# Optimization experiments

Hardware: AMD Instinct MI355X
Metric: run time of the kernel (lower is better)

## Reference

```python
import jax, jax.numpy as jnp
import numpy as np

B, S, H, KVH, D, MD = 4, 4096, 2, 1, 2, 5  # batch, seq, heads, kv heads, head_dim, model_dim
EPS, SCALE = 1e-6, 16.0


def _rmsnorm(t):
    # RMSNormNoWeight with scale=16.0 over last dim
    var = jnp.mean(t * t, axis=-1, keepdims=True)
    return SCALE * t * jax.lax.rsqrt(var + EPS)


def _rope(t, cos, sin):
    # t: (B, S, h, D); cos/sin: (S, D//2). Complex multiply on interleaved pairs.
    tr, ti = t[..., 0::2], t[..., 1::2]
    c = cos[None, :, None, :]
    s = sin[None, :, None, :]
    out_r = tr * c - ti * s
    out_i = tr * s + ti * c
    return jnp.stack([out_r, out_i], axis=-1).reshape(t.shape)


def setup_inputs() -> dict:
    key = jax.random.key(0)
    ks = jax.random.split(key, 9)
    return {
        "x": jax.random.normal(ks[0], (B, S, MD), jnp.float32),
        "freqs": jax.random.normal(ks[1], (S, D // 2), jnp.float32),
        "shared_qk_v": jax.random.normal(ks[2], (MD,), jnp.float32),
        "shared_v_v": jax.random.normal(ks[3], (MD,), jnp.float32),
        "shared_o_v": jax.random.normal(ks[4], (H * D,), jnp.float32),
        "shared_vproj_u": jax.random.normal(ks[5], (KVH * D,), jnp.float32),
        "q_u": jax.random.normal(ks[6], (H * D,), jnp.float32),
        "k_u": jax.random.normal(ks[7], (KVH * D,), jnp.float32),
        "o_u": jax.random.normal(ks[8], (MD,), jnp.float32),
    }


def reference(x, freqs, shared_qk_v, shared_v_v, shared_o_v, shared_vproj_u, q_u, k_u, o_u):
    b, s = x.shape[0], x.shape[1]
    # rank-1 projections: (x . v) outer u
    s_qk = jnp.sum(x * shared_qk_v, axis=-1, keepdims=True)  # (B,S,1) shared by q and k
    q = (s_qk * q_u).reshape(b, s, H, D)
    k = (s_qk * k_u).reshape(b, s, KVH, D)
    s_v = jnp.sum(x * shared_v_v, axis=-1, keepdims=True)
    v = (s_v * shared_vproj_u).reshape(b, s, KVH, D)
    # qk-norm + rotary
    q = _rmsnorm(q)
    k = _rmsnorm(k)
    cos, sin = jnp.cos(freqs), jnp.sin(freqs)
    q = _rope(q, cos, sin)
    k = _rope(k, cos, sin)
    # (B,h,S,D)
    q = q.transpose(0, 2, 1, 3)
    k = k.transpose(0, 2, 1, 3)
    v = v.transpose(0, 2, 1, 3)
    # GQA repeat kv heads
    k = jnp.repeat(k, H // KVH, axis=1)
    v = jnp.repeat(v, H // KVH, axis=1)
    scores = jnp.einsum('bhqd,bhkd->bhqk', q, k) / jnp.sqrt(jnp.float32(D))
    probs = jax.nn.softmax(scores, axis=-1)
    out = jnp.einsum('bhqk,bhkd->bhqd', probs, v)
    out = out.transpose(0, 2, 1, 3).reshape(b, s, H * D)
    # rank-1 output projection
    s_o = jnp.sum(out * shared_o_v, axis=-1, keepdims=True)
    return s_o * o_u  # (B,S,MODEL_DIM)
```

## Files before the change

kernel.cpp:

```cpp
#include <hip/hip_runtime.h>
#include <math.h>


#define BQ 4
#define SQ 4096
#define MDQ 5
#define EPSQ 1e-6f
#define SCALEQ 16.0f

#define BLOCK 256
#define ROWS 32
#define SPLIT 8
#define JSUB (SQ / SPLIT)
#define TILES (SQ / ROWS)

__global__ __launch_bounds__(BLOCK)
void ca_kernel(const float* __restrict__ x,
               const float* __restrict__ freqs,
               const float* __restrict__ qk_v,
               const float* __restrict__ v_v,
               const float* __restrict__ o_v,
               const float* __restrict__ vproj_u,
               const float* __restrict__ q_u,
               const float* __restrict__ k_u,
               const float* __restrict__ o_u,
               float* __restrict__ out)
{
    __shared__ float2 sPQ[SQ];
    __shared__ float  sCv[SQ];
    __shared__ float  sRed[ROWS][SPLIT][2][3];

    const int tid  = threadIdx.x;
    const int bx   = blockIdx.x;
    const int b    = bx / TILES;
    const int tile = bx % TILES;

    const float w0 = k_u[0], w1 = k_u[1];
    const float mk = 0.5f * (w0 * w0 + w1 * w1);

    const float qk0 = qk_v[0], qk1 = qk_v[1], qk2 = qk_v[2], qk3 = qk_v[3], qk4 = qk_v[4];
    const float vv0 = v_v[0],  vv1 = v_v[1],  vv2 = v_v[2],  vv3 = v_v[3],  vv4 = v_v[4];

    for (int k = 0; k < SQ / BLOCK; ++k) {
        const int j = tid + k * BLOCK;
        const float* xr = x + (size_t)(b * SQ + j) * MDQ;
        const float x0 = xr[0], x1 = xr[1], x2 = xr[2], x3 = xr[3], x4 = xr[4];
        const float a  = x0*qk0 + x1*qk1 + x2*qk2 + x3*qk3 + x4*qk4;
        const float sv = x0*vv0 + x1*vv1 + x2*vv2 + x3*vv3 + x4*vv4;
        float sj, cj;
        __sincosf(freqs[j], &sj, &cj);
        const float mu = SCALEQ * a * rsqrtf(a * a * mk + EPSQ);
        sPQ[j] = make_float2(mu * cj, mu * sj);
        sCv[j] = sv;
    }

    const int row = tid & (ROWS - 1);
    const int sp  = tid / ROWS;
    const int i   = tile * ROWS + row;

    const float u00 = q_u[0], u01 = q_u[1], u10 = q_u[2], u11 = q_u[3];
    const float m0 = 0.5f * (u00 * u00 + u01 * u01);
    const float m1 = 0.5f * (u10 * u10 + u11 * u11);
    const float A0 = u00 * w0 + u01 * w1, B0 = u01 * w0 - u00 * w1;
    const float A1 = u10 * w0 + u11 * w1, B1 = u11 * w0 - u10 * w1;

    const float* xi = x + (size_t)(b * SQ + i) * MDQ;
    const float ai = xi[0]*qk0 + xi[1]*qk1 + xi[2]*qk2 + xi[3]*qk3 + xi[4]*qk4;
    float si, ci;
    __sincosf(freqs[i], &si, &ci);
    const float lam0 = SCALEQ * ai * rsqrtf(ai * ai * m0 + EPSQ);
    const float lam1 = SCALEQ * ai * rsqrtf(ai * ai * m1 + EPSQ);
    const float isq2 = 0.70710678118654752f;
    const float al0 = lam0 * (A0 * ci - B0 * si) * isq2;
    const float be0 = lam0 * (A0 * si + B0 * ci) * isq2;
    const float al1 = lam1 * (A1 * ci - B1 * si) * isq2;
    const float be1 = lam1 * (A1 * si + B1 * ci) * isq2;

    __syncthreads();

    const float2* __restrict__ pq  = sPQ + sp * JSUB;
    const float*  __restrict__ cvp = sCv + sp * JSUB;

    float mx0 = -1e30f, mx1 = -1e30f;
#pragma unroll 8
    for (int jj = 0; jj < JSUB; ++jj) {
        const float2 v = pq[jj];
        const float sc0 = al0 * v.x + be0 * v.y;
        const float sc1 = al1 * v.x + be1 * v.y;
        mx0 = fmaxf(mx0, sc0);
        mx1 = fmaxf(mx1, sc1);
    }

    float l0 = 0.f, n0 = 0.f, l1 = 0.f, n1 = 0.f;
#pragma unroll 4
    for (int jj = 0; jj < JSUB; ++jj) {
        const float2 v = pq[jj];
        const float cv = cvp[jj];
        const float e0 = __expf(al0 * v.x + be0 * v.y - mx0);
        const float e1 = __expf(al1 * v.x + be1 * v.y - mx1);
        l0 += e0; n0 = fmaf(e0, cv, n0);
        l1 += e1; n1 = fmaf(e1, cv, n1);
    }

    sRed[row][sp][0][0] = mx0; sRed[row][sp][0][1] = l0; sRed[row][sp][0][2] = n0;
    sRed[row][sp][1][0] = mx1; sRed[row][sp][1][1] = l1; sRed[row][sp][1][2] = n1;
    __syncthreads();

    if (tid < ROWS) {
        float W[2];
#pragma unroll
        for (int h = 0; h < 2; ++h) {
            float m = -1e30f;
#pragma unroll
            for (int s = 0; s < SPLIT; ++s) m = fmaxf(m, sRed[tid][s][h][0]);
            float l = 0.f, n = 0.f;
#pragma unroll
            for (int s = 0; s < SPLIT; ++s) {
                const float c = __expf(sRed[tid][s][h][0] - m);
                l = fmaf(sRed[tid][s][h][1], c, l);
                n = fmaf(sRed[tid][s][h][2], c, n);
            }
            W[h] = n / l;
        }
        const float p0 = vproj_u[0], p1 = vproj_u[1];
        const float d0 = p0 * o_v[0] + p1 * o_v[1];
        const float d1 = p0 * o_v[2] + p1 * o_v[3];
        const float so = W[0] * d0 + W[1] * d1;

        const int ig = tile * ROWS + tid;
        float* orow = out + (size_t)(b * SQ + ig) * MDQ;
        orow[0] = so * o_u[0];
        orow[1] = so * o_u[1];
        orow[2] = so * o_u[2];
        orow[3] = so * o_u[3];
        orow[4] = so * o_u[4];
    }
}

extern "C" void kernel_launch(void* const* d_in, const int* in_sizes, int n_in,
                              void* d_out, int out_size, void* d_ws, size_t ws_size,
                              hipStream_t stream) {
    (void)in_sizes; (void)n_in; (void)d_ws; (void)ws_size; (void)out_size;
    const float* x       = (const float*)d_in[0];
    const float* freqs   = (const float*)d_in[1];
    const float* qk_v    = (const float*)d_in[2];
    const float* v_v     = (const float*)d_in[3];
    const float* o_v     = (const float*)d_in[4];
    const float* vproj_u = (const float*)d_in[5];
    const float* q_u     = (const float*)d_in[6];
    const float* k_u     = (const float*)d_in[7];
    const float* o_u     = (const float*)d_in[8];
    float* out = (float*)d_out;

    dim3 grid(BQ * TILES);
    dim3 block(BLOCK);
    hipLaunchKernelGGL(ca_kernel, grid, block, 0, stream,
                       x, freqs, qk_v, v_v, o_v, vproj_u, q_u, k_u, o_u, out);
}
```

Baseline: 112.9 us.

## Replace max pass with analytic score bound, precompute keys in a prep kernel

The per-row max pass is dropped. It is replaced by an analytic upper bound on the scores (|q|·max|k| from the rmsnorm magnitude), so the softmax becomes a single exp2 pass with the log2e factor folded into the coefficients. A separate prep kernel writes the per-key rotated values and V scalars to workspace as float4, so each main block reads them from global/L2 instead of recomputing all 4096 keys into shared memory. The tiling changes to 16 rows by 16 splits, and a fallback single-kernel path is kept for when the workspace is too small. The risk is that the bound-based shift can underflow the exps, and it adds a second launch plus global-memory traffic.

```diff
diff --git a/kernel.cpp b/kernel.cpp
--- a/kernel.cpp
+++ b/kernel.cpp
@@ -7,42 +7,174 @@
 #define MDQ 5
 #define EPSQ 1e-6f
 #define SCALEQ 16.0f
+#define L2E 1.4426950408889634f
+#define ISQ2 0.70710678118654752f
+
+__device__ __forceinline__ float fast_exp2(float x) {
+#if __has_builtin(__builtin_amdgcn_exp2f)
+    return __builtin_amdgcn_exp2f(x);
+#else
+    return __expf(x * 0.6931471805599453f);
+#endif
+}
+
+__global__ __launch_bounds__(256)
+void ca_prep(const float* __restrict__ x, const float* __restrict__ freqs,
+             const float* __restrict__ qk_v, const float* __restrict__ v_v,
+             const float* __restrict__ k_u, float4* __restrict__ pqc)
+{
+    const int idx = blockIdx.x * 256 + threadIdx.x;
+    const int j   = idx & (SQ - 1);
+
+    const float w0 = k_u[0], w1 = k_u[1];
+    const float mk = 0.5f * (w0 * w0 + w1 * w1);
+
+    const float qk0 = qk_v[0], qk1 = qk_v[1], qk2 = qk_v[2], qk3 = qk_v[3], qk4 = qk_v[4];
+    const float vv0 = v_v[0],  vv1 = v_v[1],  vv2 = v_v[2],  vv3 = v_v[3],  vv4 = v_v[4];
+
+    const float* xr = x + (size_t)idx * MDQ;
+    const float x0 = xr[0], x1 = xr[1], x2 = xr[2], x3 = xr[3], x4 = xr[4];
+    const float a  = x0*qk0 + x1*qk1 + x2*qk2 + x3*qk3 + x4*qk4;
+    const float sv = x0*vv0 + x1*vv1 + x2*vv2 + x3*vv3 + x4*vv4;
+
+    float sj, cj;
+    __sincosf(freqs[j], &sj, &cj);
+    const float mu = SCALEQ * a * rsqrtf(a * a * mk + EPSQ);
+    pqc[idx] = make_float4(mu * cj, mu * sj, sv, 0.0f);
+}
 
 #define BLOCK 256
-#define ROWS 32
-#define SPLIT 8
+#define ROWS 16
+#define SPLIT 16
 #define JSUB (SQ / SPLIT)
 #define TILES (SQ / ROWS)
 
 __global__ __launch_bounds__(BLOCK)
-void ca_kernel(const float* __restrict__ x,
-               const float* __restrict__ freqs,
-               const float* __restrict__ qk_v,
-               const float* __restrict__ v_v,
-               const float* __restrict__ o_v,
-               const float* __restrict__ vproj_u,
-               const float* __restrict__ q_u,
-               const float* __restrict__ k_u,
-               const float* __restrict__ o_u,
-               float* __restrict__ out)
+void ca_main(const float* __restrict__ x,
+             const float* __restrict__ freqs,
+             const float* __restrict__ qk_v,
+             const float* __restrict__ o_v,
+             const float* __restrict__ vproj_u,
+             const float* __restrict__ q_u,
+             const float* __restrict__ k_u,
+             const float* __restrict__ o_u,
+             const float4* __restrict__ pqc,
+             float* __restrict__ out)
 {
-    __shared__ float2 sPQ[SQ];
-    __shared__ float  sCv[SQ];
-    __shared__ float  sRed[ROWS][SPLIT][2][3];
+    __shared__ float4 sRed[ROWS][SPLIT];
 
     const int tid  = threadIdx.x;
     const int bx   = blockIdx.x;
     const int b    = bx / TILES;
     const int tile = bx % TILES;
+    const int row  = tid & (ROWS - 1);
+    const int sp   = tid / ROWS;
+    const int i    = tile * ROWS + row;
 
     const float w0 = k_u[0], w1 = k_u[1];
-    const float mk = 0.5f * (w0 * w0 + w1 * w1);
+    const float mk  = 0.5f * (w0 * w0 + w1 * w1);
+    const float Mmu = SCALEQ * rsqrtf(mk);
+
+    const float qk0 = qk_v[0], qk1 = qk_v[1], qk2 = qk_v[2], qk3 = qk_v[3], qk4 = qk_v[4];
+    const float u00 = q_u[0], u01 = q_u[1], u10 = q_u[2], u11 = q_u[3];
+    const float m0 = 0.5f * (u00 * u00 + u01 * u01);
+    const float m1 = 0.5f * (u10 * u10 + u11 * u11);
+    const float A0 = u00 * w0 + u01 * w1, B0 = u01 * w0 - u00 * w1;
+    const float A1 = u10 * w0 + u11 * w1, B1 = u11 * w0 - u10 * w1;
+
+    const float* xi = x + (size_t)(b * SQ + i) * MDQ;
+    const float ai = xi[0]*qk0 + xi[1]*qk1 + xi[2]*qk2 + xi[3]*qk3 + xi[4]*qk4;
+    float si, ci;
+    __sincosf(freqs[i], &si, &ci);
+    const float lam0 = SCALEQ * ai * rsqrtf(ai * ai * m0 + EPSQ);
+    const float lam1 = SCALEQ * ai * rsqrtf(ai * ai * m1 + EPSQ);
+
+    const float alr0 = lam0 * (A0 * ci - B0 * si) * ISQ2;
+    const float ber0 = lam0 * (A0 * si + B0 * ci) * ISQ2;
+    const float alr1 = lam1 * (A1 * ci - B1 * si) * ISQ2;
+    const float ber1 = lam1 * (A1 * si + B1 * ci) * ISQ2;
+    const float r0 = sqrtf(alr0 * alr0 + ber0 * ber0);
+    const float r1 = sqrtf(alr1 * alr1 + ber1 * ber1);
+
+    const float al0 = alr0 * L2E, be0 = ber0 * L2E, C0 = -r0 * Mmu * L2E;
+    const float al1 = alr1 * L2E, be1 = ber1 * L2E, C1 = -r1 * Mmu * L2E;
+
+    const float4* __restrict__ p = pqc + (size_t)b * SQ + sp * JSUB;
+    float l0 = 0.f, n0 = 0.f, l1 = 0.f, n1 = 0.f;
+#pragma unroll 8
+    for (int jj = 0; jj < JSUB; ++jj) {
+        const float4 v = p[jj];
+        const float s0 = fmaf(al0, v.x, fmaf(be0, v.y, C0));
+        const float s1 = fmaf(al1, v.x, fmaf(be1, v.y, C1));
+        const float e0 = fast_exp2(s0);
+        const float e1 = fast_exp2(s1);
+        l0 += e0; n0 = fmaf(e0, v.z, n0);
+        l1 += e1; n1 = fmaf(e1, v.z, n1);
+    }
+
+    sRed[row][sp] = make_float4(l0, n0, l1, n1);
+    __syncthreads();
+
+    if (tid < ROWS) {
+        float L0 = 0.f, N0 = 0.f, L1 = 0.f, N1 = 0.f;
+#pragma unroll
+        for (int s = 0; s < SPLIT; ++s) {
+            const float4 t = sRed[tid][s];
+            L0 += t.x; N0 += t.y; L1 += t.z; N1 += t.w;
+        }
+        L0 = fmaxf(L0, 1e-30f);
+        L1 = fmaxf(L1, 1e-30f);
+        const float W0 = N0 / L0, W1 = N1 / L1;
+
+        const float p0 = vproj_u[0], p1 = vproj_u[1];
+        const float d0 = p0 * o_v[0] + p1 * o_v[1];
+        const float d1 = p0 * o_v[2] + p1 * o_v[3];
+        const float so = W0 * d0 + W1 * d1;
+
+        const int ig = tile * ROWS + tid;
+        float* orow = out + (size_t)(b * SQ + ig) * MDQ;
+        orow[0] = so * o_u[0];
+        orow[1] = so * o_u[1];
+        orow[2] = so * o_u[2];
+        orow[3] = so * o_u[3];
+        orow[4] = so * o_u[4];
+    }
+}
+
+#define FROWS 32
+#define FSPLIT 8
+#define FJSUB (SQ / FSPLIT)
+#define FTILES (SQ / FROWS)
+
+__global__ __launch_bounds__(256)
+void ca_fallback(const float* __restrict__ x,
+                 const float* __restrict__ freqs,
+                 const float* __restrict__ qk_v,
+                 const float* __restrict__ v_v,
+                 const float* __restrict__ o_v,
+                 const float* __restrict__ vproj_u,
+                 const float* __restrict__ q_u,
+                 const float* __restrict__ k_u,
+                 const float* __restrict__ o_u,
+                 float* __restrict__ out)
+{
+    __shared__ float2 sPQ[SQ];
+    __shared__ float  sCv[SQ];
+    __shared__ float4 sRed[FROWS][FSPLIT];
+
+    const int tid  = threadIdx.x;
+    const int b    = blockIdx.x / FTILES;
+    const int tile = blockIdx.x % FTILES;
+
+    const float w0 = k_u[0], w1 = k_u[1];
+    const float mk  = 0.5f * (w0 * w0 + w1 * w1);
+    const float Mmu = SCALEQ * rsqrtf(mk);
 
     const float qk0 = qk_v[0], qk1 = qk_v[1], qk2 = qk_v[2], qk3 = qk_v[3], qk4 = qk_v[4];
     const float vv0 = v_v[0],  vv1 = v_v[1],  vv2 = v_v[2],  vv3 = v_v[3],  vv4 = v_v[4];
 
-    for (int k = 0; k < SQ / BLOCK; ++k) {
-        const int j = tid + k * BLOCK;
+    for (int k = 0; k < SQ / 256; ++k) {
+        const int j = tid + k * 256;
         const float* xr = x + (size_t)(b * SQ + j) * MDQ;
         const float x0 = xr[0], x1 = xr[1], x2 = xr[2], x3 = xr[3], x4 = xr[4];
         const float a  = x0*qk0 + x1*qk1 + x2*qk2 + x3*qk3 + x4*qk4;
@@ -54,9 +186,9 @@
         sCv[j] = sv;
     }
 
-    const int row = tid & (ROWS - 1);
-    const int sp  = tid / ROWS;
-    const int i   = tile * ROWS + row;
+    const int row = tid & (FROWS - 1);
+    const int sp  = tid / FROWS;
+    const int i   = tile * FROWS + row;
 
     const float u00 = q_u[0], u01 = q_u[1], u10 = q_u[2], u11 = q_u[3];
     const float m0 = 0.5f * (u00 * u00 + u01 * u01);
@@ -70,64 +202,51 @@
     __sincosf(freqs[i], &si, &ci);
     const float lam0 = SCALEQ * ai * rsqrtf(ai * ai * m0 + EPSQ);
     const float lam1 = SCALEQ * ai * rsqrtf(ai * ai * m1 + EPSQ);
-    const float isq2 = 0.70710678118654752f;
-    const float al0 = lam0 * (A0 * ci - B0 * si) * isq2;
-    const float be0 = lam0 * (A0 * si + B0 * ci) * isq2;
-    const float al1 = lam1 * (A1 * ci - B1 * si) * isq2;
-    const float be1 = lam1 * (A1 * si + B1 * ci) * isq2;
+    const float alr0 = lam0 * (A0 * ci - B0 * si) * ISQ2;
+    const float ber0 = lam0 * (A0 * si + B0 * ci) * ISQ2;
+    const float alr1 = lam1 * (A1 * ci - B1 * si) * ISQ2;
+    const float ber1 = lam1 * (A1 * si + B1 * ci) * ISQ2;
+    const float r0 = sqrtf(alr0 * alr0 + ber0 * ber0);
+    const float r1 = sqrtf(alr1 * alr1 + ber1 * ber1);
+    const float al0 = alr0 * L2E, be0 = ber0 * L2E, C0 = -r0 * Mmu * L2E;
+    const float al1 = alr1 * L2E, be1 = ber1 * L2E, C1 = -r1 * Mmu * L2E;
 
     __syncthreads();
 
-    const float2* __restrict__ pq  = sPQ + sp * JSUB;
-    const float*  __restrict__ cvp = sCv + sp * JSUB;
-
-    float mx0 = -1e30f, mx1 = -1e30f;
+    const float2* __restrict__ pq  = sPQ + sp * FJSUB;
+    const float*  __restrict__ cvp = sCv + sp * FJSUB;
+    float l0 = 0.f, n0 = 0.f, l1 = 0.f, n1 = 0.f;
 #pragma unroll 8
-    for (int jj = 0; jj < JSUB; ++jj) {
-        const float2 v = pq[jj];
-        const float sc0 = al0 * v.x + be0 * v.y;
-        const float sc1 = al1 * v.x + be1 * v.y;
-        mx0 = fmaxf(mx0, sc0);
-        mx1 = fmaxf(mx1, sc1);
-    }
-
-    float l0 = 0.f, n0 = 0.f, l1 = 0.f, n1 = 0.f;
-#pragma unroll 4
-    for (int jj = 0; jj < JSUB; ++jj) {
+    for (int jj = 0; jj < FJSUB; ++jj) {
         const float2 v = pq[jj];
         const float cv = cvp[jj];
-        const float e0 = __expf(al0 * v.x + be0 * v.y - mx0);
-        const float e1 = __expf(al1 * v.x + be1 * v.y - mx1);
+        const float s0 = fmaf(al0, v.x, fmaf(be0, v.y, C0));
+        const float s1 = fmaf(al1, v.x, fmaf(be1, v.y, C1));
+        const float e0 = fast_exp2(s0);
+        const float e1 = fast_exp2(s1);
         l0 += e0; n0 = fmaf(e0, cv, n0);
         l1 += e1; n1 = fmaf(e1, cv, n1);
     }
 
-    sRed[row][sp][0][0] = mx0; sRed[row][sp][0][1] = l0; sRed[row][sp][0][2] = n0;
-    sRed[row][sp][1][0] = mx1; sRed[row][sp][1][1] = l1; sRed[row][sp][1][2] = n1;
+    sRed[row][sp] = make_float4(l0, n0, l1, n1);
     __syncthreads();
 
-    if (tid < ROWS) {
-        float W[2];
+    if (tid < FROWS) {
+        float L0 = 0.f, N0 = 0.f, L1 = 0.f, N1 = 0.f;
 #pragma unroll
-        for (int h = 0; h < 2; ++h) {
-            float m = -1e30f;
-#pragma unroll
-            for (int s = 0; s < SPLIT; ++s) m = fmaxf(m, sRed[tid][s][h][0]);
-            float l = 0.f, n = 0.f;
-#pragma unroll
-            for (int s = 0; s < SPLIT; ++s) {
-                const float c = __expf(sRed[tid][s][h][0] - m);
-                l = fmaf(sRed[tid][s][h][1], c, l);
-                n = fmaf(sRed[tid][s][h][2], c, n);
-            }
-            W[h] = n / l;
+        for (int s = 0; s < FSPLIT; ++s) {
+            const float4 t = sRed[tid][s];
+            L0 += t.x; N0 += t.y; L1 += t.z; N1 += t.w;
         }
+        L0 = fmaxf(L0, 1e-30f);
+        L1 = fmaxf(L1, 1e-30f);
+        const float W0 = N0 / L0, W1 = N1 / L1;
         const float p0 = vproj_u[0], p1 = vproj_u[1];
         const float d0 = p0 * o_v[0] + p1 * o_v[1];
         const float d1 = p0 * o_v[2] + p1 * o_v[3];
-        const float so = W[0] * d0 + W[1] * d1;
-
-        const int ig = tile * ROWS + tid;
+        const float so = W0 * d0 + W1 * d1;
+
+        const int ig = tile * FROWS + tid;
         float* orow = out + (size_t)(b * SQ + ig) * MDQ;
         orow[0] = so * o_u[0];
         orow[1] = so * o_u[1];
@@ -140,7 +259,7 @@
 extern "C" void kernel_launch(void* const* d_in, const int* in_sizes, int n_in,
                               void* d_out, int out_size, void* d_ws, size_t ws_size,
                               hipStream_t stream) {
-    (void)in_sizes; (void)n_in; (void)d_ws; (void)ws_size; (void)out_size;
+    (void)in_sizes; (void)n_in; (void)out_size;
     const float* x       = (const float*)d_in[0];
     const float* freqs   = (const float*)d_in[1];
     const float* qk_v    = (const float*)d_in[2];
@@ -152,8 +271,15 @@
     const float* o_u     = (const float*)d_in[8];
     float* out = (float*)d_out;
 
-    dim3 grid(BQ * TILES);
-    dim3 block(BLOCK);
-    hipLaunchKernelGGL(ca_kernel, grid, block, 0, stream,
-                       x, freqs, qk_v, v_v, o_v, vproj_u, q_u, k_u, o_u, out);
-}
+    const size_t pqc_bytes = (size_t)BQ * SQ * sizeof(float4);
+    if (ws_size >= pqc_bytes) {
+        float4* pqc = (float4*)d_ws;
+        hipLaunchKernelGGL(ca_prep, dim3(BQ * SQ / 256), dim3(256), 0, stream,
+                           x, freqs, qk_v, v_v, k_u, pqc);
+        hipLaunchKernelGGL(ca_main, dim3(BQ * TILES), dim3(BLOCK), 0, stream,
+                           x, freqs, qk_v, o_v, vproj_u, q_u, k_u, o_u, pqc, out);
+    } else {
+        hipLaunchKernelGGL(ca_fallback, dim3(BQ * FTILES), dim3(256), 0, stream,
+                           x, freqs, qk_v, v_v, o_v, vproj_u, q_u, k_u, o_u, out);
+    }
+}
```

Result: faster. 107.7 us (-4.6%).
